# Optimization experiments

Hardware: AMD Instinct MI355X
Metric: run time of the kernel (lower is better)

The kernel has to match this reference:

```python
import jax, jax.numpy as jnp
import numpy as np

N_NODES = 100000
N_EDGES = 600000
NODE_DIM = 128
EDGE_DIM = 16
OUT_DIM = 128


def setup_inputs() -> dict:
    key = jax.random.key(0)
    k1, k2, k3, k4 = jax.random.split(key, 4)
    x = jax.random.normal(k1, (N_NODES, NODE_DIM), dtype=jnp.float32)
    edge_index = jax.random.randint(k2, (2, N_EDGES), 0, N_NODES, dtype=jnp.int64)
    edge_attr = jax.random.normal(k3, (N_EDGES, EDGE_DIM), dtype=jnp.float32)
    in_dim = 2 * NODE_DIM + EDGE_DIM
    # Linear layer params (Kaiming-uniform-like scale)
    lim = 1.0 / np.sqrt(in_dim)
    W = jax.random.uniform(k4, (in_dim, OUT_DIM), minval=-lim, maxval=lim, dtype=jnp.float32)
    b = jnp.zeros((OUT_DIM,), dtype=jnp.float32)
    return {"x": x, "edge_index": edge_index, "edge_attr": edge_attr, "W": W, "b": b}


def reference(x, edge_index, edge_attr, W, b):
    # h_ij = Linear([h_i, h_j, x_ij])
    h_i = x[edge_index[0]]            # [E, node_dim]
    h_j = x[edge_index[1]]            # [E, node_dim]
    # Split the GEMM over the concat blocks to avoid materializing [E, 2D+F]
    W_i, W_j, W_e = W[:NODE_DIM], W[NODE_DIM:2 * NODE_DIM], W[2 * NODE_DIM:]
    out = h_i @ W_i + h_j @ W_j + edge_attr @ W_e + b
    return out  # [E, out_dim]
```

## Files before the change

### kernel.cpp

```cpp
#include <hip/hip_runtime.h>
#include <cstdint>
#include <cstddef>

#define NE 600000
#define NN 100000

typedef __attribute__((ext_vector_type(8)))  __bf16        bf16x8;
typedef __attribute__((ext_vector_type(16))) float         f32x16;
typedef __attribute__((ext_vector_type(8)))  unsigned short u16x8;

__device__ inline unsigned short f2bf(float f) {
    unsigned int u = __builtin_bit_cast(unsigned int, f);
    u += 0x7fffu + ((u >> 16) & 1u);
    return (unsigned short)(u >> 16);
}

__global__ void pack_w(const float* __restrict__ W, unsigned short* __restrict__ Wp) {
    int t = blockIdx.x * 256 + threadIdx.x;
    if (t >= 272 * 128) return;
    int k = t >> 7, col = t & 127;
    Wp[((k >> 3) * 128 + col) * 8 + (k & 7)] = f2bf(W[t]);
}

__global__ void cvt_x(const float* __restrict__ x, unsigned short* __restrict__ xb) {
    size_t t = (size_t)(blockIdx.x * 256 + threadIdx.x) * 8;
    float4 a = *(const float4*)(x + t);
    float4 b = *(const float4*)(x + t + 4);
    u16x8 o;
    o[0] = f2bf(a.x); o[1] = f2bf(a.y); o[2] = f2bf(a.z); o[3] = f2bf(a.w);
    o[4] = f2bf(b.x); o[5] = f2bf(b.y); o[6] = f2bf(b.z); o[7] = f2bf(b.w);
    *(u16x8*)(xb + t) = o;
}

template <bool USE_BF16X>
__global__ __launch_bounds__(256, 2) void edge_mm(
    const void* __restrict__ xsrc,
    const unsigned short* __restrict__ Wp,
    const int* __restrict__ ei,
    const float* __restrict__ ea,
    const float* __restrict__ bias,
    float* __restrict__ out)
{
    __shared__ unsigned short Wl[32 * 128 * 8];

    {
        const uint4* Wg = (const uint4*)Wp;
        uint4* Ws = (uint4*)Wl;
#pragma unroll
        for (int i = 0; i < 16; ++i)
            Ws[threadIdx.x + 256 * i] = Wg[threadIdx.x + 256 * i];
    }

    const int lane = threadIdx.x & 63;
    const int wave = threadIdx.x >> 6;
    const int r = lane & 31;
    const int h = lane >> 5;
    const long ebase = (long)blockIdx.x * 128 + wave * 32;

    __syncthreads();
    if (ebase >= NE) return;

    const int e = (int)ebase + r;
    const int src = ei[e];
    const int dst = ei[NE + e];

    f32x16 acc[4];
#pragma unroll
    for (int t = 0; t < 4; ++t)
#pragma unroll
        for (int i = 0; i < 16; ++i) acc[t][i] = 0.f;

    const bf16x8* Wv = (const bf16x8*)Wl;

#pragma unroll
    for (int s = 0; s < 8; ++s) {
        bf16x8 a;
        if (USE_BF16X) {
            const bf16x8* ax = (const bf16x8*)((const unsigned short*)xsrc + (size_t)src * 128);
            a = ax[2 * s + h];
        } else {
            const float4* ax = (const float4*)((const float*)xsrc + (size_t)src * 128);
            float4 p = ax[(2 * s + h) * 2], q = ax[(2 * s + h) * 2 + 1];
            u16x8 o;
            o[0] = f2bf(p.x); o[1] = f2bf(p.y); o[2] = f2bf(p.z); o[3] = f2bf(p.w);
            o[4] = f2bf(q.x); o[5] = f2bf(q.y); o[6] = f2bf(q.z); o[7] = f2bf(q.w);
            a = __builtin_bit_cast(bf16x8, o);
        }
        const int S = s;
#pragma unroll
        for (int t = 0; t < 4; ++t) {
            bf16x8 b = Wv[(2 * S + h) * 128 + t * 32 + r];
            acc[t] = __builtin_amdgcn_mfma_f32_32x32x16_bf16(a, b, acc[t], 0, 0, 0);
        }
    }

#pragma unroll
    for (int s = 0; s < 8; ++s) {
        bf16x8 a;
        if (USE_BF16X) {
            const bf16x8* ax = (const bf16x8*)((const unsigned short*)xsrc + (size_t)dst * 128);
            a = ax[2 * s + h];
        } else {
            const float4* ax = (const float4*)((const float*)xsrc + (size_t)dst * 128);
            float4 p = ax[(2 * s + h) * 2], q = ax[(2 * s + h) * 2 + 1];
            u16x8 o;
            o[0] = f2bf(p.x); o[1] = f2bf(p.y); o[2] = f2bf(p.z); o[3] = f2bf(p.w);
            o[4] = f2bf(q.x); o[5] = f2bf(q.y); o[6] = f2bf(q.z); o[7] = f2bf(q.w);
            a = __builtin_bit_cast(bf16x8, o);
        }
        const int S = 8 + s;
#pragma unroll
        for (int t = 0; t < 4; ++t) {
            bf16x8 b = Wv[(2 * S + h) * 128 + t * 32 + r];
            acc[t] = __builtin_amdgcn_mfma_f32_32x32x16_bf16(a, b, acc[t], 0, 0, 0);
        }
    }

    {
        const float4* ae = (const float4*)(ea + (size_t)e * 16);
        float4 p = ae[2 * h], q = ae[2 * h + 1];
        u16x8 o;
        o[0] = f2bf(p.x); o[1] = f2bf(p.y); o[2] = f2bf(p.z); o[3] = f2bf(p.w);
        o[4] = f2bf(q.x); o[5] = f2bf(q.y); o[6] = f2bf(q.z); o[7] = f2bf(q.w);
        bf16x8 a = __builtin_bit_cast(bf16x8, o);
        const bf16x8* Wg = (const bf16x8*)Wp;
#pragma unroll
        for (int t = 0; t < 4; ++t) {
            bf16x8 b = Wg[(32 + h) * 128 + t * 32 + r];
            acc[t] = __builtin_amdgcn_mfma_f32_32x32x16_bf16(a, b, acc[t], 0, 0, 0);
        }
    }

    float* orow = out + (size_t)ebase * 128;
#pragma unroll
    for (int t = 0; t < 4; ++t) {
        float bv = bias[t * 32 + r];
#pragma unroll
        for (int i = 0; i < 16; ++i) {
            int row = (i & 3) + 8 * (i >> 2) + 4 * h;
            orow[(size_t)row * 128 + t * 32 + r] = acc[t][i] + bv;
        }
    }
}

extern "C" void kernel_launch(void* const* d_in, const int* in_sizes, int n_in,
                              void* d_out, int out_size, void* d_ws, size_t ws_size,
                              hipStream_t stream) {
    const float* x  = (const float*)d_in[0];
    const int*   ei = (const int*)d_in[1];
    const float* ea = (const float*)d_in[2];
    const float* W  = (const float*)d_in[3];
    const float* b  = (const float*)d_in[4];
    float* out = (float*)d_out;

    unsigned short* Wp = (unsigned short*)d_ws;
    unsigned short* xb = (unsigned short*)((char*)d_ws + 69632);
    const size_t need = 69632 + (size_t)NN * 128 * 2;

    hipLaunchKernelGGL(pack_w, dim3(136), dim3(256), 0, stream, W, Wp);

    if (ws_size >= need) {
        hipLaunchKernelGGL(cvt_x, dim3(6250), dim3(256), 0, stream, x, xb);
        hipLaunchKernelGGL((edge_mm<true>), dim3(4688), dim3(256), 0, stream,
                           (const void*)xb, Wp, ei, ea, b, out);
    } else {
        hipLaunchKernelGGL((edge_mm<false>), dim3(4688), dim3(256), 0, stream,
                           (const void*)x, Wp, ei, ea, b, out);
    }
}
```

Before: 442.8 us.

## Gather node rows directly into LDS asynchronously and read weights from global

The main edge kernel now gathers the src and dst bf16 node rows straight into per-wave LDS buffers with global_load_lds, using an XOR swizzle on the 16-byte chunks to avoid bank conflicts. It waits on the vmcnt counter so the src-half MFMAs can start while the dst gathers are still in flight. The per-block copy of the 64KB weights into LDS and the __syncthreads are dropped, and weights are read from global/L2 instead. This trades LDS weight reuse for lower LDS use and more overlap. It depends on a hand-coded waitcnt encoding being correct.

```diff
diff --git a/kernel.cpp b/kernel.cpp
--- a/kernel.cpp
+++ b/kernel.cpp
@@ -5,8 +5,8 @@
 #define NE 600000
 #define NN 100000
 
-typedef __attribute__((ext_vector_type(8)))  __bf16        bf16x8;
-typedef __attribute__((ext_vector_type(16))) float         f32x16;
+typedef __attribute__((ext_vector_type(8)))  __bf16         bf16x8;
+typedef __attribute__((ext_vector_type(16))) float          f32x16;
 typedef __attribute__((ext_vector_type(8)))  unsigned short u16x8;
 
 __device__ inline unsigned short f2bf(float f) {
@@ -32,9 +32,113 @@
     *(u16x8*)(xb + t) = o;
 }
 
-template <bool USE_BF16X>
-__global__ __launch_bounds__(256, 2) void edge_mm(
-    const void* __restrict__ xsrc,
+#define WAIT_VM(n) do { asm volatile("" ::: "memory");                      \
+                        __builtin_amdgcn_s_waitcnt(0x0F70 | (n));           \
+                        asm volatile("" ::: "memory"); } while (0)
+
+__global__ __launch_bounds__(256, 2) void edge_mm2(
+    const unsigned short* __restrict__ xb,
+    const unsigned short* __restrict__ Wp,
+    const int* __restrict__ ei,
+    const float* __restrict__ ea,
+    const float* __restrict__ bias,
+    float* __restrict__ out)
+{
+    __shared__ __attribute__((aligned(16))) unsigned short Abuf[4][2][32][128];
+
+    const int lane = threadIdx.x & 63;
+    const int wave = threadIdx.x >> 6;
+    const int r  = lane & 31;
+    const int h  = lane >> 5;
+    const int g4 = lane >> 4;
+    const int sl = lane & 15;
+    const int ebase = blockIdx.x * 128 + wave * 32;
+    if (ebase >= NE) return;
+    const int e = ebase + r;
+
+#pragma unroll
+    for (int i = 0; i < 8; ++i) {
+        int row = 4 * i + g4;
+        int nidx = ei[ebase + row];
+        const unsigned short* gs = xb + (size_t)nidx * 128 + ((sl ^ (row & 15)) << 3);
+        __builtin_amdgcn_global_load_lds(
+            (const __attribute__((address_space(1))) void*)gs,
+            (__attribute__((address_space(3))) void*)&Abuf[wave][0][4 * i][0],
+            16, 0, 0);
+    }
+#pragma unroll
+    for (int i = 0; i < 8; ++i) {
+        int row = 4 * i + g4;
+        int nidx = ei[NE + ebase + row];
+        const unsigned short* gs = xb + (size_t)nidx * 128 + ((sl ^ (row & 15)) << 3);
+        __builtin_amdgcn_global_load_lds(
+            (const __attribute__((address_space(1))) void*)gs,
+            (__attribute__((address_space(3))) void*)&Abuf[wave][1][4 * i][0],
+            16, 0, 0);
+    }
+
+    const float4* ae = (const float4*)(ea + (size_t)e * 16);
+    float4 p = ae[2 * h], q = ae[2 * h + 1];
+
+    f32x16 acc[4];
+#pragma unroll
+    for (int t = 0; t < 4; ++t)
+#pragma unroll
+        for (int i = 0; i < 16; ++i) acc[t][i] = 0.f;
+
+    const bf16x8* Wg = (const bf16x8*)Wp;
+    const int rm = r & 15;
+
+    WAIT_VM(8);
+#pragma unroll
+    for (int S = 0; S < 8; ++S) {
+        int kb = 2 * S + h;
+        bf16x8 a = *(const bf16x8*)&Abuf[wave][0][r][(kb ^ rm) << 3];
+#pragma unroll
+        for (int t = 0; t < 4; ++t) {
+            bf16x8 b = Wg[kb * 128 + t * 32 + r];
+            acc[t] = __builtin_amdgcn_mfma_f32_32x32x16_bf16(a, b, acc[t], 0, 0, 0);
+        }
+    }
+
+    WAIT_VM(0);
+#pragma unroll
+    for (int S = 0; S < 8; ++S) {
+        int kb = 2 * S + h;
+        bf16x8 a = *(const bf16x8*)&Abuf[wave][1][r][(kb ^ rm) << 3];
+#pragma unroll
+        for (int t = 0; t < 4; ++t) {
+            bf16x8 b = Wg[(16 + kb) * 128 + t * 32 + r];
+            acc[t] = __builtin_amdgcn_mfma_f32_32x32x16_bf16(a, b, acc[t], 0, 0, 0);
+        }
+    }
+
+    {
+        u16x8 o;
+        o[0] = f2bf(p.x); o[1] = f2bf(p.y); o[2] = f2bf(p.z); o[3] = f2bf(p.w);
+        o[4] = f2bf(q.x); o[5] = f2bf(q.y); o[6] = f2bf(q.z); o[7] = f2bf(q.w);
+        bf16x8 a = __builtin_bit_cast(bf16x8, o);
+#pragma unroll
+        for (int t = 0; t < 4; ++t) {
+            bf16x8 b = Wg[(32 + h) * 128 + t * 32 + r];
+            acc[t] = __builtin_amdgcn_mfma_f32_32x32x16_bf16(a, b, acc[t], 0, 0, 0);
+        }
+    }
+
+    float* orow = out + (size_t)ebase * 128;
+#pragma unroll
+    for (int t = 0; t < 4; ++t) {
+        float bv = bias[t * 32 + r];
+#pragma unroll
+        for (int i = 0; i < 16; ++i) {
+            int row = (i & 3) + 8 * (i >> 2) + 4 * h;
+            orow[(size_t)row * 128 + t * 32 + r] = acc[t][i] + bv;
+        }
+    }
+}
+
+__global__ __launch_bounds__(256, 2) void edge_mm_fb(
+    const float* __restrict__ x,
     const unsigned short* __restrict__ Wp,
     const int* __restrict__ ei,
     const float* __restrict__ ea,
@@ -42,7 +146,6 @@
     float* __restrict__ out)
 {
     __shared__ unsigned short Wl[32 * 128 * 8];
-
     {
         const uint4* Wg = (const uint4*)Wp;
         uint4* Ws = (uint4*)Wl;
@@ -50,78 +153,47 @@
         for (int i = 0; i < 16; ++i)
             Ws[threadIdx.x + 256 * i] = Wg[threadIdx.x + 256 * i];
     }
-
     const int lane = threadIdx.x & 63;
     const int wave = threadIdx.x >> 6;
     const int r = lane & 31;
     const int h = lane >> 5;
     const long ebase = (long)blockIdx.x * 128 + wave * 32;
-
     __syncthreads();
     if (ebase >= NE) return;
-
     const int e = (int)ebase + r;
     const int src = ei[e];
     const int dst = ei[NE + e];
-
     f32x16 acc[4];
 #pragma unroll
     for (int t = 0; t < 4; ++t)
 #pragma unroll
         for (int i = 0; i < 16; ++i) acc[t][i] = 0.f;
-
     const bf16x8* Wv = (const bf16x8*)Wl;
-
-#pragma unroll
-    for (int s = 0; s < 8; ++s) {
-        bf16x8 a;
-        if (USE_BF16X) {
-            const bf16x8* ax = (const bf16x8*)((const unsigned short*)xsrc + (size_t)src * 128);
-            a = ax[2 * s + h];
-        } else {
-            const float4* ax = (const float4*)((const float*)xsrc + (size_t)src * 128);
-            float4 p = ax[(2 * s + h) * 2], q = ax[(2 * s + h) * 2 + 1];
+#pragma unroll
+    for (int ph = 0; ph < 2; ++ph) {
+        int node = ph ? dst : src;
+#pragma unroll
+        for (int s = 0; s < 8; ++s) {
+            const float4* ax = (const float4*)(x + (size_t)node * 128);
+            float4 pp = ax[(2 * s + h) * 2], qq = ax[(2 * s + h) * 2 + 1];
             u16x8 o;
-            o[0] = f2bf(p.x); o[1] = f2bf(p.y); o[2] = f2bf(p.z); o[3] = f2bf(p.w);
-            o[4] = f2bf(q.x); o[5] = f2bf(q.y); o[6] = f2bf(q.z); o[7] = f2bf(q.w);
-            a = __builtin_bit_cast(bf16x8, o);
-        }
-        const int S = s;
-#pragma unroll
-        for (int t = 0; t < 4; ++t) {
-            bf16x8 b = Wv[(2 * S + h) * 128 + t * 32 + r];
-            acc[t] = __builtin_amdgcn_mfma_f32_32x32x16_bf16(a, b, acc[t], 0, 0, 0);
-        }
-    }
-
-#pragma unroll
-    for (int s = 0; s < 8; ++s) {
-        bf16x8 a;
-        if (USE_BF16X) {
-            const bf16x8* ax = (const bf16x8*)((const unsigned short*)xsrc + (size_t)dst * 128);
-            a = ax[2 * s + h];
-        } else {
-            const float4* ax = (const float4*)((const float*)xsrc + (size_t)dst * 128);
-            float4 p = ax[(2 * s + h) * 2], q = ax[(2 * s + h) * 2 + 1];
-            u16x8 o;
-            o[0] = f2bf(p.x); o[1] = f2bf(p.y); o[2] = f2bf(p.z); o[3] = f2bf(p.w);
-            o[4] = f2bf(q.x); o[5] = f2bf(q.y); o[6] = f2bf(q.z); o[7] = f2bf(q.w);
-            a = __builtin_bit_cast(bf16x8, o);
-        }
-        const int S = 8 + s;
-#pragma unroll
-        for (int t = 0; t < 4; ++t) {
-            bf16x8 b = Wv[(2 * S + h) * 128 + t * 32 + r];
-            acc[t] = __builtin_amdgcn_mfma_f32_32x32x16_bf16(a, b, acc[t], 0, 0, 0);
-        }
-    }
-
+            o[0] = f2bf(pp.x); o[1] = f2bf(pp.y); o[2] = f2bf(pp.z); o[3] = f2bf(pp.w);
+            o[4] = f2bf(qq.x); o[5] = f2bf(qq.y); o[6] = f2bf(qq.z); o[7] = f2bf(qq.w);
+            bf16x8 a = __builtin_bit_cast(bf16x8, o);
+            int S = ph * 8 + s;
+#pragma unroll
+            for (int t = 0; t < 4; ++t) {
+                bf16x8 b = Wv[(2 * S + h) * 128 + t * 32 + r];
+                acc[t] = __builtin_amdgcn_mfma_f32_32x32x16_bf16(a, b, acc[t], 0, 0, 0);
+            }
+        }
+    }
     {
         const float4* ae = (const float4*)(ea + (size_t)e * 16);
-        float4 p = ae[2 * h], q = ae[2 * h + 1];
+        float4 pp = ae[2 * h], qq = ae[2 * h + 1];
         u16x8 o;
-        o[0] = f2bf(p.x); o[1] = f2bf(p.y); o[2] = f2bf(p.z); o[3] = f2bf(p.w);
-        o[4] = f2bf(q.x); o[5] = f2bf(q.y); o[6] = f2bf(q.z); o[7] = f2bf(q.w);
+        o[0] = f2bf(pp.x); o[1] = f2bf(pp.y); o[2] = f2bf(pp.z); o[3] = f2bf(pp.w);
+        o[4] = f2bf(qq.x); o[5] = f2bf(qq.y); o[6] = f2bf(qq.z); o[7] = f2bf(qq.w);
         bf16x8 a = __builtin_bit_cast(bf16x8, o);
         const bf16x8* Wg = (const bf16x8*)Wp;
 #pragma unroll
@@ -130,7 +202,6 @@
             acc[t] = __builtin_amdgcn_mfma_f32_32x32x16_bf16(a, b, acc[t], 0, 0, 0);
         }
     }
-
     float* orow = out + (size_t)ebase * 128;
 #pragma unroll
     for (int t = 0; t < 4; ++t) {
@@ -161,10 +232,10 @@
 
     if (ws_size >= need) {
         hipLaunchKernelGGL(cvt_x, dim3(6250), dim3(256), 0, stream, x, xb);
-        hipLaunchKernelGGL((edge_mm<true>), dim3(4688), dim3(256), 0, stream,
-                           (const void*)xb, Wp, ei, ea, b, out);
+        hipLaunchKernelGGL(edge_mm2, dim3(4688), dim3(256), 0, stream,
+                           xb, Wp, ei, ea, b, out);
     } else {
-        hipLaunchKernelGGL((edge_mm<false>), dim3(4688), dim3(256), 0, stream,
-                           (const void*)x, Wp, ei, ea, b, out);
-    }
-}
+        hipLaunchKernelGGL(edge_mm_fb, dim3(4688), dim3(256), 0, stream,
+                           x, Wp, ei, ea, b, out);
+    }
+}
```

After: 434.8 us. About the same (-1.8%).
